# Kernel tuning notes

Measured on AMD Instinct MI355X. Metric: run time of the kernel, lower is better.

Reference implementation:

```python
import jax, jax.numpy as jnp
import numpy as np

B, S, D = 4, 2048, 2048   # batch, seq, embed
E, R = 64, 64             # experts, expert_rank
INIT_SCALE = 0.02


def setup_inputs() -> dict:
    key = jax.random.key(0)
    k_x, k_m, k_up, k_dn = jax.random.split(key, 4)
    x = jax.random.normal(k_x, (B, S, D), dtype=jnp.float32)
    expert_mask = jax.random.uniform(k_m, (B, S, E), dtype=jnp.float32)
    # up_proj weight, out_first=True: [experts, rank, embed]
    w_up = jax.random.normal(k_up, (E, R, D), dtype=jnp.float32) * INIT_SCALE
    # down_proj weight, out_first=True: [embed, experts, rank]
    w_down = jax.random.normal(k_dn, (D, E, R), dtype=jnp.float32) * INIT_SCALE
    return {"x": x, "expert_mask": expert_mask, "w_up": w_up, "w_down": w_down}


def reference(x, expert_mask, w_up, w_down):
    # up projection: [B,S,D] x [E,R,D] -> [B,S,E,R]
    h = jnp.einsum("bsd,erd->bser", x, w_up)
    h = jax.nn.silu(h)
    # mask inactive experts (broadcast over rank)
    h = h * expert_mask[:, :, :, None]
    # down projection: [B,S,E,R] x [D,E,R] -> [B,S,D]
    out = jnp.einsum("bser,der->bsd", h, w_down)
    return out
```

## Files before the change

kernel.cpp:

```cpp
#include <hip/hip_runtime.h>
#include <hip/hip_bf16.h>

typedef unsigned short u16;
typedef unsigned int   u32;
typedef __attribute__((ext_vector_type(8))) short  s16x8;
typedef __attribute__((ext_vector_type(4))) float  f32x4;
typedef __attribute__((ext_vector_type(4))) unsigned short u16x4;

#define MT    8192
#define DE    2048
#define NEXP  64
#define ERDIM 4096

__device__ __forceinline__ u16 to_bf16(float f) {
  u32 u = __builtin_bit_cast(u32, f);
  u32 r = u + 0x7fffu + ((u >> 16) & 1u);
  return (u16)(r >> 16);
}

__global__ void cvt_f32_bf16(const float* __restrict__ in, u16* __restrict__ out, int n) {
  const int stride = gridDim.x * blockDim.x;
  for (int i = blockIdx.x * blockDim.x + threadIdx.x; i * 4 < n; i += stride) {
    const float4 v = *reinterpret_cast<const float4*>(in + (size_t)i * 4);
    u16x4 o;
    o.x = to_bf16(v.x); o.y = to_bf16(v.y); o.z = to_bf16(v.z); o.w = to_bf16(v.w);
    *reinterpret_cast<u16x4*>(out + (size_t)i * 4) = o;
  }
}

#define GLDS(gp, lp) __builtin_amdgcn_global_load_lds(                        \
    (const __attribute__((address_space(1))) void*)(gp),                      \
    (__attribute__((address_space(3))) void*)(lp), 16, 0, 0)

#define BAR() do { asm volatile("" ::: "memory");                             \
                   __builtin_amdgcn_s_barrier();                              \
                   asm volatile("" ::: "memory"); } while (0)

template<int FUSE>
__global__ __launch_bounds__(512) void gemm_bt(
    const u16* __restrict__ A, const u16* __restrict__ Bm,
    const float* __restrict__ mask, void* __restrict__ Cout,
    const int M, const int N, const int K)
{
  constexpr int BM = 256, BN = 256, BK = 32;
  __shared__ __align__(16) u16 lds[65536];

  const int nbn = N / BN;
  const int nwg = (int)gridDim.x;
  const int cpx = nwg >> 3;
  const int bid = (int)blockIdx.x;
  const int swz = (bid & 7) * cpx + (bid >> 3);
  const int bm = (swz / nbn) * BM;
  const int bn = (swz % nbn) * BN;

  const int tid  = (int)threadIdx.x;
  const int lane = tid & 63;
  const int w    = tid >> 6;
  const int wr   = w >> 2;
  const int wc   = w & 3;

  const int fr = lane & 15;
  const int cp = (lane >> 4) ^ ((lane >> 1) & 3);

  const int lr = lane >> 2;
  const int cl = (lane & 3) ^ ((lane >> 3) & 3);
  const int c0 = 2 * w, c1 = 2 * w + 1;
  const u16* aS0 = A  + (size_t)(bm + c0 * 16 + lr) * K + cl * 8;
  const u16* aS1 = A  + (size_t)(bm + c1 * 16 + lr) * K + cl * 8;
  const u16* bS0 = Bm + (size_t)(bn + c0 * 16 + lr) * K + cl * 8;
  const u16* bS1 = Bm + (size_t)(bn + c1 * 16 + lr) * K + cl * 8;

  const int NT = K / BK;

  f32x4 acc[8][4] = {};

  GLDS(aS0,      lds + 0 * 16384 +        c0 * 512);
  GLDS(aS1,      lds + 0 * 16384 +        c1 * 512);
  GLDS(bS0,      lds + 0 * 16384 + 8192 + c0 * 512);
  GLDS(bS1,      lds + 0 * 16384 + 8192 + c1 * 512);
  GLDS(aS0 + BK, lds + 1 * 16384 +        c0 * 512);
  GLDS(aS1 + BK, lds + 1 * 16384 +        c1 * 512);
  GLDS(bS0 + BK, lds + 1 * 16384 + 8192 + c0 * 512);
  GLDS(bS1 + BK, lds + 1 * 16384 + 8192 + c1 * 512);
  asm volatile("s_waitcnt vmcnt(4)" ::: "memory");
  BAR();

  for (int t = 0; t < NT; ++t) {
    const int slot = t & 3;
    const u16* sA = lds + slot * 16384;
    const u16* sB = lds + slot * 16384 + 8192;
    const int s2 = (t + 2) & 3;
    u16* dst = lds + s2 * 16384;
    const bool st = (t + 2 < NT);
    const size_t koff = (size_t)(t + 2) * BK;

    s16x8 bfr[4];
#pragma unroll
    for (int mh = 0; mh < 2; ++mh) {
      s16x8 afr[4];
#pragma unroll
      for (int m = 0; m < 4; ++m)
        afr[m] = *reinterpret_cast<const s16x8*>(
            &sA[(wr * 128 + (mh * 4 + m) * 16 + fr) * 32 + cp * 8]);
      if (mh == 0) {
#pragma unroll
        for (int n = 0; n < 4; ++n)
          bfr[n] = *reinterpret_cast<const s16x8*>(
              &sB[(wc * 64 + n * 16 + fr) * 32 + cp * 8]);
        if (st) {
          GLDS(aS0 + koff, dst +        c0 * 512);
          GLDS(aS1 + koff, dst +        c1 * 512);
        }
      } else {
        if (st) {
          GLDS(bS0 + koff, dst + 8192 + c0 * 512);
          GLDS(bS1 + koff, dst + 8192 + c1 * 512);
        }
      }
      BAR();
      __builtin_amdgcn_s_setprio(1);
#pragma unroll
      for (int m = 0; m < 4; ++m)
#pragma unroll
        for (int n = 0; n < 4; ++n)
          acc[mh * 4 + m][n] = __builtin_amdgcn_mfma_f32_16x16x32_bf16(
              afr[m], bfr[n], acc[mh * 4 + m][n], 0, 0, 0);
      __builtin_amdgcn_s_setprio(0);
      if (mh == 0) {
        BAR();
      } else {
        if (t + 2 < NT)      asm volatile("s_waitcnt vmcnt(4)" ::: "memory");
        else if (t + 1 < NT) asm volatile("s_waitcnt vmcnt(0)" ::: "memory");
        if (t + 1 < NT) BAR();
      }
    }
  }

  const int rgrp = (lane >> 4) * 4;
  if (FUSE) {
    u16* H = (u16*)Cout;
    const int ew = (bn + wc * 64) >> 6;
#pragma unroll
    for (int m = 0; m < 8; ++m) {
#pragma unroll
      for (int j = 0; j < 4; ++j) {
        const int grow = bm + wr * 128 + m * 16 + rgrp + j;
        const float mv = mask[(size_t)grow * NEXP + ew];
#pragma unroll
        for (int n = 0; n < 4; ++n) {
          const int gcol = bn + wc * 64 + n * 16 + fr;
          float v = acc[m][n][j];
          v = v / (1.0f + __expf(-v));
          H[(size_t)grow * N + gcol] = to_bf16(v * mv);
        }
      }
    }
  } else {
    float* O = (float*)Cout;
#pragma unroll
    for (int m = 0; m < 8; ++m) {
#pragma unroll
      for (int j = 0; j < 4; ++j) {
        const int grow = bm + wr * 128 + m * 16 + rgrp + j;
#pragma unroll
        for (int n = 0; n < 4; ++n) {
          const int gcol = bn + wc * 64 + n * 16 + fr;
          O[(size_t)grow * N + gcol] = acc[m][n][j];
        }
      }
    }
  }
}

extern "C" void kernel_launch(void* const* d_in, const int* in_sizes, int n_in,
                              void* d_out, int out_size, void* d_ws, size_t ws_size,
                              hipStream_t stream) {
  const float* x     = (const float*)d_in[0];
  const float* emask = (const float*)d_in[1];
  const float* w_up  = (const float*)d_in[2];
  const float* w_dn  = (const float*)d_in[3];
  float* out = (float*)d_out;

  const size_t need = ((size_t)MT * DE + (size_t)ERDIM * DE + (size_t)DE * ERDIM +
                       (size_t)MT * ERDIM) * sizeof(u16);
  if (ws_size < need) return;

  u16* xb  = (u16*)d_ws;
  u16* wub = xb  + (size_t)MT * DE;
  u16* wdb = wub + (size_t)ERDIM * DE;
  u16* hb  = wdb + (size_t)DE * ERDIM;

  hipLaunchKernelGGL(cvt_f32_bf16, dim3(2048), dim3(256), 0, stream, x,    xb,  MT * DE);
  hipLaunchKernelGGL(cvt_f32_bf16, dim3(1024), dim3(256), 0, stream, w_up, wub, ERDIM * DE);
  hipLaunchKernelGGL(cvt_f32_bf16, dim3(1024), dim3(256), 0, stream, w_dn, wdb, DE * ERDIM);

  hipLaunchKernelGGL((gemm_bt<1>), dim3((MT / 256) * (ERDIM / 256)), dim3(512), 0, stream,
                     xb, wub, emask, (void*)hb, MT, ERDIM, DE);
  hipLaunchKernelGGL((gemm_bt<0>), dim3((MT / 256) * (DE / 256)), dim3(512), 0, stream,
                     hb, wdb, nullptr, (void*)out, MT, DE, ERDIM);
}
```

Baseline: 309.9 us.

## Deepen GEMM LDS prefetch to three stages and drop intra-iteration barriers

The bf16 GEMM main loop now keeps three K-tiles in flight across its four LDS slots instead of two. It also replaces the three barriers per K-step with a single end-of-iteration barrier, paired with staged vmcnt waits. K becomes a template parameter so the loop trip count is known at compile time, and the loop is unrolled by four. The launch bounds now request two blocks per CU, which caps register use. With a 128-entry accumulator per thread that cap could force spills, and the 128 KB LDS buffer likely prevents two blocks from being resident anyway.

```diff
diff --git a/kernel.cpp b/kernel.cpp
--- a/kernel.cpp
+++ b/kernel.cpp
@@ -36,13 +36,14 @@
                    __builtin_amdgcn_s_barrier();                              \
                    asm volatile("" ::: "memory"); } while (0)
 
-template<int FUSE>
-__global__ __launch_bounds__(512) void gemm_bt(
+template<int FUSE, int K>
+__global__ __launch_bounds__(512, 2) void gemm_bt(
     const u16* __restrict__ A, const u16* __restrict__ Bm,
     const float* __restrict__ mask, void* __restrict__ Cout,
-    const int M, const int N, const int K)
+    const int M, const int N)
 {
   constexpr int BM = 256, BN = 256, BK = 32;
+  constexpr int NT = K / BK;
   __shared__ __align__(16) u16 lds[65536];
 
   const int nbn = N / BN;
@@ -70,70 +71,76 @@
   const u16* bS0 = Bm + (size_t)(bn + c0 * 16 + lr) * K + cl * 8;
   const u16* bS1 = Bm + (size_t)(bn + c1 * 16 + lr) * K + cl * 8;
 
-  const int NT = K / BK;
-
   f32x4 acc[8][4] = {};
 
-  GLDS(aS0,      lds + 0 * 16384 +        c0 * 512);
-  GLDS(aS1,      lds + 0 * 16384 +        c1 * 512);
-  GLDS(bS0,      lds + 0 * 16384 + 8192 + c0 * 512);
-  GLDS(bS1,      lds + 0 * 16384 + 8192 + c1 * 512);
-  GLDS(aS0 + BK, lds + 1 * 16384 +        c0 * 512);
-  GLDS(aS1 + BK, lds + 1 * 16384 +        c1 * 512);
-  GLDS(bS0 + BK, lds + 1 * 16384 + 8192 + c0 * 512);
-  GLDS(bS1 + BK, lds + 1 * 16384 + 8192 + c1 * 512);
-  asm volatile("s_waitcnt vmcnt(4)" ::: "memory");
+#pragma unroll
+  for (int t = 0; t < 3; ++t) {
+    u16* dst = lds + t * 16384;
+    GLDS(aS0 + t * BK, dst +        c0 * 512);
+    GLDS(aS1 + t * BK, dst +        c1 * 512);
+    GLDS(bS0 + t * BK, dst + 8192 + c0 * 512);
+    GLDS(bS1 + t * BK, dst + 8192 + c1 * 512);
+  }
+  asm volatile("s_waitcnt vmcnt(8)" ::: "memory");
   BAR();
 
+#pragma unroll 4
   for (int t = 0; t < NT; ++t) {
     const int slot = t & 3;
     const u16* sA = lds + slot * 16384;
     const u16* sB = lds + slot * 16384 + 8192;
-    const int s2 = (t + 2) & 3;
-    u16* dst = lds + s2 * 16384;
-    const bool st = (t + 2 < NT);
-    const size_t koff = (size_t)(t + 2) * BK;
-
-    s16x8 bfr[4];
-#pragma unroll
-    for (int mh = 0; mh < 2; ++mh) {
-      s16x8 afr[4];
-#pragma unroll
-      for (int m = 0; m < 4; ++m)
-        afr[m] = *reinterpret_cast<const s16x8*>(
-            &sA[(wr * 128 + (mh * 4 + m) * 16 + fr) * 32 + cp * 8]);
-      if (mh == 0) {
-#pragma unroll
-        for (int n = 0; n < 4; ++n)
-          bfr[n] = *reinterpret_cast<const s16x8*>(
-              &sB[(wc * 64 + n * 16 + fr) * 32 + cp * 8]);
-        if (st) {
-          GLDS(aS0 + koff, dst +        c0 * 512);
-          GLDS(aS1 + koff, dst +        c1 * 512);
-        }
-      } else {
-        if (st) {
-          GLDS(bS0 + koff, dst + 8192 + c0 * 512);
-          GLDS(bS1 + koff, dst + 8192 + c1 * 512);
-        }
-      }
-      BAR();
-      __builtin_amdgcn_s_setprio(1);
-#pragma unroll
-      for (int m = 0; m < 4; ++m)
-#pragma unroll
-        for (int n = 0; n < 4; ++n)
-          acc[mh * 4 + m][n] = __builtin_amdgcn_mfma_f32_16x16x32_bf16(
-              afr[m], bfr[n], acc[mh * 4 + m][n], 0, 0, 0);
-      __builtin_amdgcn_s_setprio(0);
-      if (mh == 0) {
-        BAR();
-      } else {
-        if (t + 2 < NT)      asm volatile("s_waitcnt vmcnt(4)" ::: "memory");
-        else if (t + 1 < NT) asm volatile("s_waitcnt vmcnt(0)" ::: "memory");
-        if (t + 1 < NT) BAR();
-      }
-    }
+    u16* dst = lds + ((t + 3) & 3) * 16384;
+    const bool st = (t + 3 < NT);
+    const size_t koff = (size_t)(t + 3) * BK;
+
+    s16x8 afr[4], bfr[4];
+#pragma unroll
+    for (int m = 0; m < 4; ++m)
+      afr[m] = *reinterpret_cast<const s16x8*>(
+          &sA[(wr * 128 + m * 16 + fr) * 32 + cp * 8]);
+#pragma unroll
+    for (int n = 0; n < 4; ++n)
+      bfr[n] = *reinterpret_cast<const s16x8*>(
+          &sB[(wc * 64 + n * 16 + fr) * 32 + cp * 8]);
+    if (st) {
+      GLDS(aS0 + koff, dst +        c0 * 512);
+      GLDS(aS1 + koff, dst +        c1 * 512);
+    }
+    __builtin_amdgcn_s_setprio(1);
+#pragma unroll
+    for (int m = 0; m < 4; ++m)
+#pragma unroll
+      for (int n = 0; n < 4; ++n)
+        acc[m][n] = __builtin_amdgcn_mfma_f32_16x16x32_bf16(
+            afr[m], bfr[n], acc[m][n], 0, 0, 0);
+    __builtin_amdgcn_s_setprio(0);
+
+    s16x8 afr2[4];
+#pragma unroll
+    for (int m = 0; m < 4; ++m)
+      afr2[m] = *reinterpret_cast<const s16x8*>(
+          &sA[(wr * 128 + (4 + m) * 16 + fr) * 32 + cp * 8]);
+    if (st) {
+      GLDS(bS0 + koff, dst + 8192 + c0 * 512);
+      GLDS(bS1 + koff, dst + 8192 + c1 * 512);
+    }
+    __builtin_amdgcn_s_setprio(1);
+#pragma unroll
+    for (int m = 0; m < 4; ++m)
+#pragma unroll
+      for (int n = 0; n < 4; ++n)
+        acc[4 + m][n] = __builtin_amdgcn_mfma_f32_16x16x32_bf16(
+            afr2[m], bfr[n], acc[4 + m][n], 0, 0, 0);
+    __builtin_amdgcn_s_setprio(0);
+
+    if (t + 3 < NT) {
+      asm volatile("s_waitcnt vmcnt(8)" ::: "memory");
+    } else if (t + 2 < NT) {
+      asm volatile("s_waitcnt vmcnt(4)" ::: "memory");
+    } else if (t + 1 < NT) {
+      asm volatile("s_waitcnt vmcnt(0)" ::: "memory");
+    }
+    if (t + 1 < NT) BAR();
   }
 
   const int rgrp = (lane >> 4) * 4;
@@ -194,8 +201,8 @@
   hipLaunchKernelGGL(cvt_f32_bf16, dim3(1024), dim3(256), 0, stream, w_up, wub, ERDIM * DE);
   hipLaunchKernelGGL(cvt_f32_bf16, dim3(1024), dim3(256), 0, stream, w_dn, wdb, DE * ERDIM);
 
-  hipLaunchKernelGGL((gemm_bt<1>), dim3((MT / 256) * (ERDIM / 256)), dim3(512), 0, stream,
-                     xb, wub, emask, (void*)hb, MT, ERDIM, DE);
-  hipLaunchKernelGGL((gemm_bt<0>), dim3((MT / 256) * (DE / 256)), dim3(512), 0, stream,
-                     hb, wdb, nullptr, (void*)out, MT, DE, ERDIM);
-}
+  hipLaunchKernelGGL((gemm_bt<1, DE>), dim3((MT / 256) * (ERDIM / 256)), dim3(512), 0, stream,
+                     xb, wub, emask, (void*)hb, MT, ERDIM);
+  hipLaunchKernelGGL((gemm_bt<0, ERDIM>), dim3((MT / 256) * (DE / 256)), dim3(512), 0, stream,
+                     hb, wdb, nullptr, (void*)out, MT, DE);
+}
```

After: 281.8 us. 9.1% less time.
